# Performance work log

Hardware: AMD Instinct MI355X
Metric: run time of the kernel (lower is better)

Reference implementation:

```python
import jax, jax.numpy as jnp
import numpy as np

D_MODEL = 1024
NUM_HEADS = 16
D_K = D_MODEL // NUM_HEADS
EPS = 1e-6


def setup_inputs() -> dict:
    key = jax.random.key(0)
    ks = jax.random.split(key, 16)
    B, S = 2, 2048
    sc_in = 1.0 / np.sqrt(D_MODEL)
    sc_na = 1.0 / np.sqrt(D_K)
    inp = {
        "Q": jax.random.normal(ks[0], (B, S, D_MODEL), jnp.float32),
        "K": jax.random.normal(ks[1], (B, S, D_MODEL), jnp.float32),
        "V": jax.random.normal(ks[2], (B, S, D_MODEL), jnp.float32),
        "mask": jax.random.randint(ks[3], (1, 1, S, S), 0, 2, jnp.int32),
        # projection weights stored [in, out] (math-equivalent to torch Linear)
        "wq": jax.random.normal(ks[4], (D_MODEL, D_MODEL), jnp.float32) * sc_in,
        "bq": jnp.zeros((D_MODEL,), jnp.float32),
        "wk": jax.random.normal(ks[5], (D_MODEL, D_MODEL), jnp.float32) * sc_in,
        "bk": jnp.zeros((D_MODEL,), jnp.float32),
        "wv": jax.random.normal(ks[6], (D_MODEL, D_MODEL), jnp.float32) * sc_in,
        "bv": jnp.zeros((D_MODEL,), jnp.float32),
        "wo": jax.random.normal(ks[7], (D_MODEL, D_MODEL), jnp.float32) * sc_in,
        "bo": jnp.zeros((D_MODEL,), jnp.float32),
        # NeuralAttention score-fn params (per-head-dim transforms)
        "wnq": jax.random.normal(ks[8], (D_K, D_K), jnp.float32) * sc_na,
        "bnq": jnp.zeros((D_K,), jnp.float32),
        "wnk": jax.random.normal(ks[9], (D_K, D_K), jnp.float32) * sc_na,
        "bnk": jnp.zeros((D_K,), jnp.float32),
        "temperature": jnp.ones((NUM_HEADS, 1, 1), jnp.float32),
        "gamma": jnp.ones((D_MODEL,), jnp.float32),
    }
    return inp


def _split_heads(x):
    B, S, _ = x.shape
    return x.reshape(B, S, NUM_HEADS, D_K).transpose(0, 2, 1, 3)  # [B,H,S,dk]


def reference(Q, K, V, mask, wq, bq, wk, bk, wv, bv, wo, bo,
              wnq, bnq, wnk, bnk, temperature, gamma):
    B, S, _ = Q.shape
    q = _split_heads(Q @ wq + bq)  # [B,H,S,dk]
    k = _split_heads(K @ wk + bk)
    v = _split_heads(V @ wv + bv)
    # NeuralAttention: nonlinear per-token feature maps, then contraction
    qf = jnp.tanh(q @ wnq + bnq)
    kf = jnp.tanh(k @ wnk + bnk)
    scores = jnp.einsum('bhqd,bhkd->bhqk', qf, kf) / jnp.sqrt(jnp.float32(D_K))
    scores = scores / temperature  # [H,1,1] broadcasts over [B,H,S,S]
    scores = jnp.where(mask == 0, jnp.float32(-1e9), scores)
    attn = jax.nn.softmax(scores, axis=-1)
    ctx = jnp.einsum('bhqk,bhkd->bhqd', attn, v)
    out = ctx.transpose(0, 2, 1, 3).reshape(B, S, D_MODEL) @ wo + bo
    # RMSNorm
    rms = jax.lax.rsqrt(jnp.mean(out * out, axis=-1, keepdims=True) + EPS)
    return out * rms * gamma
```

## Files before the change

kernel.cpp:

```cpp
#include <hip/hip_runtime.h>
#include <hip/hip_bf16.h>
#include <math.h>

#define S_LEN 2048
#define BATCH 2
#define NH 16
#define DK 64
#define DM 1024
#define BS (BATCH * S_LEN)
#define BHS (BATCH * NH * S_LEN)
#define TRP 72
#define PSTR 72

using bf16x8  = __attribute__((ext_vector_type(8))) __bf16;
using floatx4 = __attribute__((ext_vector_type(4))) float;
using ushort4v = __attribute__((ext_vector_type(4))) unsigned short;

extern "C" __device__ float __ocml_exp2_f32(float);

__device__ __forceinline__ unsigned short f2bf(float f) {
    union { float f; unsigned u; } v; v.f = f;
    unsigned r = v.u + 0x7fffu + ((v.u >> 16) & 1u);
    return (unsigned short)(r >> 16);
}

__device__ __forceinline__ unsigned cvt_pk_bf16(float a, float b) {
    unsigned r;
    asm("v_cvt_pk_bf16_f32 %0, %1, %2" : "=v"(r) : "v"(a), "v"(b));
    return r;
}

__device__ __forceinline__ float fast_tanh(float x) {
    float e = __ocml_exp2_f32(x * 2.8853900817779268f);
    return 1.0f - 2.0f / (e + 1.0f);
}

__device__ __forceinline__ void gl2lds16(const void* g, void* l) {
    __builtin_amdgcn_global_load_lds(
        (__attribute__((address_space(1))) void*)(uintptr_t)g,
        (__attribute__((address_space(3))) void*)(uintptr_t)l,
        16, 0, 0);
}

__global__ void k_convert(const float* __restrict__ q, const float* __restrict__ k,
                          const float* __restrict__ v,
                          unsigned short* __restrict__ qb, unsigned short* __restrict__ kb,
                          unsigned short* __restrict__ vb) {
    const int N4 = BS * DM / 4;
    int i = blockIdx.x * 256 + threadIdx.x;
    int which = i / N4;
    int off = i - which * N4;
    const floatx4* src = (const floatx4*)(which == 0 ? q : which == 1 ? k : v);
    unsigned short* dst = which == 0 ? qb : which == 1 ? kb : vb;
    floatx4 x = src[off];
    ushort4v o;
    unsigned p01 = cvt_pk_bf16(x[0], x[1]);
    unsigned p23 = cvt_pk_bf16(x[2], x[3]);
    o[0] = (unsigned short)p01; o[1] = (unsigned short)(p01 >> 16);
    o[2] = (unsigned short)p23; o[3] = (unsigned short)(p23 >> 16);
    ((ushort4v*)dst)[off] = o;
}

__global__ void k_transpose(const float* s0, const float* s1, const float* s2, const float* s3,
                            unsigned short* d0, unsigned short* d1, unsigned short* d2,
                            unsigned short* d3, int n) {
    int z = blockIdx.z;
    const float* src = z == 0 ? s0 : z == 1 ? s1 : z == 2 ? s2 : s3;
    unsigned short* dst = z == 0 ? d0 : z == 1 ? d1 : z == 2 ? d2 : d3;
    __shared__ unsigned short tile[32][33];
    int tx = threadIdx.x & 31, ty = threadIdx.x >> 5;
#pragma unroll
    for (int i = 0; i < 4; i++) {
        int y = blockIdx.y * 32 + i * 8 + ty;
        tile[i * 8 + ty][tx] = f2bf(src[(size_t)y * n + blockIdx.x * 32 + tx]);
    }
    __syncthreads();
#pragma unroll
    for (int i = 0; i < 4; i++) {
        int r = blockIdx.x * 32 + i * 8 + ty;
        dst[(size_t)r * n + blockIdx.y * 32 + tx] = tile[tx][i * 8 + ty];
    }
}

__global__ void k_maskpack(const int* __restrict__ mask, unsigned int* __restrict__ mb) {
    int t = blockIdx.x * 256 + threadIdx.x;
    int row = t >> 6, w = t & 63;
    const int* p = mask + (size_t)row * S_LEN + w * 32;
    unsigned bits = 0;
#pragma unroll
    for (int i = 0; i < 32; i++) bits |= (p[i] != 0 ? 1u : 0u) << i;
    mb[t] = bits;
}

__global__ __launch_bounds__(256) void k_gemm_qkv(
    const unsigned short* __restrict__ Qb, const unsigned short* __restrict__ Kb,
    const unsigned short* __restrict__ Vb,
    const unsigned short* __restrict__ Wqt, const unsigned short* __restrict__ Wkt,
    const unsigned short* __restrict__ Wvt,
    const float* __restrict__ bq, const float* __restrict__ bk, const float* __restrict__ bv,
    unsigned short* __restrict__ qh, unsigned short* __restrict__ kh,
    unsigned short* __restrict__ vfrag) {
    const int K = DM;
    int z = blockIdx.z;
    const unsigned short* A  = z == 0 ? Qb  : z == 1 ? Kb  : Vb;
    const unsigned short* Wt = z == 0 ? Wqt : z == 1 ? Wkt : Wvt;
    const float* bias        = z == 0 ? bq  : z == 1 ? bk  : bv;
    int m0 = blockIdx.y * 128, n0 = blockIdx.x * 128;
    __shared__ unsigned short As[128 * 32];
    __shared__ unsigned short Bs[128 * 32];
    __shared__ unsigned short Tr[4][32 * TRP];
    int tid = threadIdx.x;
    int lane = tid & 63, wid = tid >> 6;
    int wy = wid >> 1, wx = wid & 1;
    int l16 = lane & 15, quad = lane >> 4;

    floatx4 acc[4][4] = {};

    for (int kt = 0; kt < K / 32; kt++) {
        int kk = kt * 32;
#pragma unroll
        for (int i = 0; i < 2; i++) {
            int c = i * 256 + tid;
            int row = c >> 2, seg = c & 3;
            gl2lds16(A + (size_t)(m0 + row) * K + kk + seg * 8, &As[c * 8]);
            gl2lds16(Wt + (size_t)(n0 + row) * K + kk + seg * 8, &Bs[c * 8]);
        }
        __syncthreads();
        bf16x8 af[4], bf[4];
#pragma unroll
        for (int mi = 0; mi < 4; mi++)
            af[mi] = *(const bf16x8*)&As[(wy * 64 + mi * 16 + l16) * 32 + quad * 8];
#pragma unroll
        for (int ni = 0; ni < 4; ni++)
            bf[ni] = *(const bf16x8*)&Bs[(wx * 64 + ni * 16 + l16) * 32 + quad * 8];
#pragma unroll
        for (int mi = 0; mi < 4; mi++)
#pragma unroll
            for (int ni = 0; ni < 4; ni++)
                acc[mi][ni] = __builtin_amdgcn_mfma_f32_16x16x32_bf16(af[mi], bf[ni], acc[mi][ni], 0, 0, 0);
        __syncthreads();
    }

    float bvv[4];
#pragma unroll
    for (int ni = 0; ni < 4; ni++) bvv[ni] = bias[n0 + wx * 64 + ni * 16 + l16];
    int head = (n0 + wx * 64) >> 6;
    int mbase = m0 + wy * 64;
    int b = mbase >> 11;
    unsigned short* tw = &Tr[wid][0];

    if (z < 2) {
        unsigned short* out = z == 0 ? qh : kh;
        size_t rowbase = (size_t)((b * NH + head) * S_LEN + (mbase & (S_LEN - 1))) * DK;
#pragma unroll
        for (int hh = 0; hh < 2; hh++) {
#pragma unroll
            for (int mi2 = 0; mi2 < 2; mi2++) {
                int mi = hh * 2 + mi2;
#pragma unroll
                for (int ni = 0; ni < 4; ni++) {
                    unsigned p01 = cvt_pk_bf16(acc[mi][ni][0] + bvv[ni], acc[mi][ni][1] + bvv[ni]);
                    unsigned p23 = cvt_pk_bf16(acc[mi][ni][2] + bvv[ni], acc[mi][ni][3] + bvv[ni]);
                    int ad = (mi2 * 16 + quad * 4) * TRP + ni * 16 + l16;
                    tw[ad] = (unsigned short)p01;
                    tw[ad + TRP] = (unsigned short)(p01 >> 16);
                    tw[ad + 2 * TRP] = (unsigned short)p23;
                    tw[ad + 3 * TRP] = (unsigned short)(p23 >> 16);
                }
            }
#pragma unroll
            for (int c = 0; c < 4; c++) {
                int g = c * 64 + lane;
                int ml = g >> 3, dc = g & 7;
                bf16x8 vv = *(const bf16x8*)&tw[ml * TRP + dc * 8];
                *(bf16x8*)&out[rowbase + (size_t)(hh * 32 + ml) * DK + dc * 8] = vv;
            }
        }
    } else {
        int kt2 = (mbase & (S_LEN - 1)) >> 6;
        size_t tilebase = ((size_t)(b * NH + head) * 32 + kt2) * 4096;
#pragma unroll
        for (int hh = 0; hh < 2; hh++) {
#pragma unroll
            for (int ni2 = 0; ni2 < 2; ni2++) {
                int ni = hh * 2 + ni2;
#pragma unroll
                for (int mi = 0; mi < 4; mi++) {
                    unsigned p01 = cvt_pk_bf16(acc[mi][ni][0] + bvv[ni], acc[mi][ni][1] + bvv[ni]);
                    unsigned p23 = cvt_pk_bf16(acc[mi][ni][2] + bvv[ni], acc[mi][ni][3] + bvv[ni]);
                    int ad = (ni2 * 16 + l16) * TRP + mi * 16 + quad * 4;
                    *(unsigned*)&tw[ad] = p01;
                    *(unsigned*)&tw[ad + 2] = p23;
                }
            }
#pragma unroll
            for (int c = 0; c < 4; c++) {
                int g = c * 64 + lane;
                int lt = g & 63;
                int qt = lt >> 4, l16t = lt & 15;
                int ad = ((c >> 1) * 16 + l16t) * TRP + (c & 1) * 32 + qt * 8;
                bf16x8 vv = *(const bf16x8*)&tw[ad];
                *(bf16x8*)&vfrag[tilebase + (size_t)(4 * hh + c) * 512 + lt * 8] = vv;
            }
        }
    }
}

__global__ __launch_bounds__(256) void k_gemm_out(const unsigned short* __restrict__ A,
                                                  const unsigned short* __restrict__ Wt,
                                                  const float* __restrict__ bias,
                                                  float* __restrict__ out_f32) {
    const int K = DM;
    int m0 = blockIdx.y * 128, n0 = blockIdx.x * 128;
    __shared__ unsigned short As[128 * 32];
    __shared__ unsigned short Bs[128 * 32];
    int tid = threadIdx.x;
    int lane = tid & 63, wid = tid >> 6;
    int wy = wid >> 1, wx = wid & 1;
    int l16 = lane & 15, quad = lane >> 4;

    floatx4 acc[4][4] = {};

    for (int kt = 0; kt < K / 32; kt++) {
        int kk = kt * 32;
#pragma unroll
        for (int i = 0; i < 2; i++) {
            int c = i * 256 + tid;
            int row = c >> 2, seg = c & 3;
            gl2lds16(A + (size_t)(m0 + row) * K + kk + seg * 8, &As[c * 8]);
            gl2lds16(Wt + (size_t)(n0 + row) * K + kk + seg * 8, &Bs[c * 8]);
        }
        __syncthreads();
        bf16x8 af[4], bf[4];
#pragma unroll
        for (int mi = 0; mi < 4; mi++)
            af[mi] = *(const bf16x8*)&As[(wy * 64 + mi * 16 + l16) * 32 + quad * 8];
#pragma unroll
        for (int ni = 0; ni < 4; ni++)
            bf[ni] = *(const bf16x8*)&Bs[(wx * 64 + ni * 16 + l16) * 32 + quad * 8];
#pragma unroll
        for (int mi = 0; mi < 4; mi++)
#pragma unroll
            for (int ni = 0; ni < 4; ni++)
                acc[mi][ni] = __builtin_amdgcn_mfma_f32_16x16x32_bf16(af[mi], bf[ni], acc[mi][ni], 0, 0, 0);
        __syncthreads();
    }

#pragma unroll
    for (int mi = 0; mi < 4; mi++) {
#pragma unroll
        for (int ni = 0; ni < 4; ni++) {
            int col = n0 + wx * 64 + ni * 16 + l16;
            float bvv = bias[col];
#pragma unroll
            for (int r = 0; r < 4; r++) {
                int row = m0 + wy * 64 + mi * 16 + quad * 4 + r;
                out_f32[(size_t)row * DM + col] = acc[mi][ni][r] + bvv;
            }
        }
    }
}

__global__ __launch_bounds__(256) void k_feature(const unsigned short* __restrict__ qh,
                                                 const unsigned short* __restrict__ kh,
                                                 const unsigned short* __restrict__ wnqt,
                                                 const unsigned short* __restrict__ wnkt,
                                                 const float* __restrict__ bnq,
                                                 const float* __restrict__ bnk,
                                                 const float* __restrict__ temp,
                                                 unsigned short* __restrict__ qfb,
                                                 unsigned short* __restrict__ kfrag) {
    int zy = blockIdx.y;
    const unsigned short* src = zy == 0 ? qh : kh;
    const unsigned short* wt = zy == 0 ? wnqt : wnkt;
    const float* bias = zy == 0 ? bnq : bnk;

    __shared__ unsigned short Tr[64 * TRP];
    int tid = threadIdx.x, lane = tid & 63, wid = tid >> 6;
    int l16 = lane & 15, quad = lane >> 4;
    int row0 = blockIdx.x * 64;
    int bh = row0 >> 11, h = bh & 15;
    float sc = (zy == 0) ? 1.4426950408889634f / (8.0f * temp[h]) : 1.0f;

    bf16x8 af[2];
#pragma unroll
    for (int ks = 0; ks < 2; ks++)
        af[ks] = *(const bf16x8*)(src + (size_t)(row0 + wid * 16 + l16) * DK + ks * 32 + quad * 8);

    floatx4 acc[4] = {};
#pragma unroll
    for (int ni = 0; ni < 4; ni++) {
#pragma unroll
        for (int ks = 0; ks < 2; ks++) {
            bf16x8 bfr = *(const bf16x8*)(wt + (size_t)(ni * 16 + l16) * DK + ks * 32 + quad * 8);
            acc[ni] = __builtin_amdgcn_mfma_f32_16x16x32_bf16(af[ks], bfr, acc[ni], 0, 0, 0);
        }
    }
#pragma unroll
    for (int ni = 0; ni < 4; ni++) {
        float bv = bias[ni * 16 + l16];
        float t0 = fast_tanh(acc[ni][0] + bv) * sc;
        float t1 = fast_tanh(acc[ni][1] + bv) * sc;
        float t2 = fast_tanh(acc[ni][2] + bv) * sc;
        float t3 = fast_tanh(acc[ni][3] + bv) * sc;
        unsigned p01 = cvt_pk_bf16(t0, t1);
        unsigned p23 = cvt_pk_bf16(t2, t3);
        int ad = (wid * 16 + quad * 4) * TRP + ni * 16 + l16;
        Tr[ad] = (unsigned short)p01;
        Tr[ad + TRP] = (unsigned short)(p01 >> 16);
        Tr[ad + 2 * TRP] = (unsigned short)p23;
        Tr[ad + 3 * TRP] = (unsigned short)(p23 >> 16);
    }
    __syncthreads();
    if (zy == 0) {
#pragma unroll
        for (int c = 0; c < 2; c++) {
            int g = c * 256 + tid;
            int ml = g >> 3, dc = g & 7;
            bf16x8 vv = *(const bf16x8*)&Tr[ml * TRP + dc * 8];
            *(bf16x8*)&qfb[(size_t)(row0 + ml) * DK + dc * 8] = vv;
        }
    } else {
        int kt = (row0 & (S_LEN - 1)) >> 6;
        size_t tb = ((size_t)bh * 32 + kt) * 4096;
#pragma unroll
        for (int c = 0; c < 2; c++) {
            int F = c * 256 + tid;
            int i = F >> 6, lt = F & 63;
            int qt = lt >> 4, lt16 = lt & 15;
            int ad = ((i >> 1) * 16 + lt16) * TRP + (i & 1) * 32 + qt * 8;
            bf16x8 vv = *(const bf16x8*)&Tr[ad];
            *(bf16x8*)&kfrag[tb + (size_t)i * 512 + lt * 8] = vv;
        }
    }
}

__global__ __launch_bounds__(256, 4) void k_attn(const unsigned short* __restrict__ qf,
                                                 const unsigned short* __restrict__ kfr,
                                                 const unsigned short* __restrict__ vfr,
                                                 const unsigned long long* __restrict__ mb64,
                                                 unsigned short* __restrict__ ctx) {
    int tid = threadIdx.x, lane = tid & 63, wid = tid >> 6;
    int l16 = lane & 15, quad = lane >> 4;
    int bh = blockIdx.y;
    int b = bh >> 4, h = bh & 15;
    int q0 = blockIdx.x * 64 + wid * 16;

    const unsigned short* qfb = qf + (size_t)bh * S_LEN * DK;
    const unsigned short* kbase = kfr + (size_t)bh * 32 * 4096;
    const unsigned short* vbase = vfr + (size_t)bh * 32 * 4096;

    __shared__ unsigned short Kbuf[2][4096];
    __shared__ unsigned short Plds[4][16 * PSTR];
    unsigned short* myP = Plds[wid];

    bf16x8 aq[2];
#pragma unroll
    for (int ks = 0; ks < 2; ks++)
        aq[ks] = *(const bf16x8*)(qfb + (size_t)(q0 + l16) * DK + ks * 32 + quad * 8);

    gl2lds16(kbase + tid * 8, &Kbuf[0][tid * 8]);
    gl2lds16(kbase + 2048 + tid * 8, &Kbuf[0][2048 + tid * 8]);

    floatx4 oacc[4] = {};
    float l_part[4] = {0.f, 0.f, 0.f, 0.f};
    const unsigned long long* mrow = mb64 + (size_t)(q0 + quad * 4) * 32;

    for (int kt = 0; kt < S_LEN / 64; kt++) {
        __syncthreads();
        int nb = (kt + 1) & 1;
        const unsigned short* kn = kbase + (size_t)((kt + 1) & 31) * 4096;
        gl2lds16(kn + tid * 8, &Kbuf[nb][tid * 8]);
        gl2lds16(kn + 2048 + tid * 8, &Kbuf[nb][2048 + tid * 8]);
        const unsigned short* vt = vbase + (size_t)kt * 4096 + lane * 8;
        bf16x8 vf[8];
#pragma unroll
        for (int i = 0; i < 8; i++) vf[i] = *(const bf16x8*)(vt + i * 512);
        unsigned wlo[4], whi[4];
#pragma unroll
        for (int r = 0; r < 4; r++) {
            unsigned long long m = mrow[r * 32 + kt];
            wlo[r] = (unsigned)(m >> l16);
            whi[r] = (unsigned)(m >> (l16 + 32));
        }
        const unsigned short* kb = &Kbuf[kt & 1][lane * 8];
        bf16x8 kf8[8];
#pragma unroll
        for (int i = 0; i < 8; i++) kf8[i] = *(const bf16x8*)(kb + i * 512);
        floatx4 sf[4];
#pragma unroll
        for (int ni = 0; ni < 4; ni++) {
            floatx4 z = {};
            z = __builtin_amdgcn_mfma_f32_16x16x32_bf16(aq[0], kf8[ni * 2], z, 0, 0, 0);
            z = __builtin_amdgcn_mfma_f32_16x16x32_bf16(aq[1], kf8[ni * 2 + 1], z, 0, 0, 0);
            sf[ni] = z;
        }
#pragma unroll
        for (int ni2 = 0; ni2 < 2; ni2++) {
#pragma unroll
            for (int r = 0; r < 4; r++) {
                unsigned wv = ni2 ? whi[r] : wlo[r];
                float sA = (wv & 1u) ? sf[2 * ni2][r] : -23.0f;
                float sB = (wv & 0x10000u) ? sf[2 * ni2 + 1][r] : -23.0f;
                float pA = __ocml_exp2_f32(sA);
                float pB = __ocml_exp2_f32(sB);
                l_part[r] += pA + pB;
                unsigned pk = cvt_pk_bf16(pA, pB);
                int ad = (quad * 4 + r) * PSTR + ni2 * 32 + l16;
                myP[ad] = (unsigned short)pk;
                myP[ad + 16] = (unsigned short)(pk >> 16);
            }
        }
        bf16x8 pa[2];
#pragma unroll
        for (int ks = 0; ks < 2; ks++)
            pa[ks] = *(const bf16x8*)&myP[l16 * PSTR + ks * 32 + quad * 8];
#pragma unroll
        for (int ni = 0; ni < 4; ni++) {
            oacc[ni] = __builtin_amdgcn_mfma_f32_16x16x32_bf16(pa[0], vf[ni * 2], oacc[ni], 0, 0, 0);
            oacc[ni] = __builtin_amdgcn_mfma_f32_16x16x32_bf16(pa[1], vf[ni * 2 + 1], oacc[ni], 0, 0, 0);
        }
    }
#pragma unroll
    for (int r = 0; r < 4; r++) {
#pragma unroll
        for (int off = 1; off < 16; off <<= 1)
            l_part[r] += __shfl_xor(l_part[r], off, 16);
    }
    float inv[4];
#pragma unroll
    for (int r = 0; r < 4; r++) inv[r] = 1.0f / l_part[r];
#pragma unroll
    for (int ni = 0; ni < 4; ni++) {
        int d = ni * 16 + l16;
#pragma unroll
        for (int r = 0; r < 4; r++) {
            int s = q0 + quad * 4 + r;
            ctx[(size_t)(b * S_LEN + s) * DM + h * DK + d] = f2bf(oacc[ni][r] * inv[r]);
        }
    }
}

__global__ __launch_bounds__(256) void k_rmsnorm(const float* __restrict__ x,
                                                 const float* __restrict__ gamma,
                                                 float* __restrict__ out) {
    int row = blockIdx.x, tid = threadIdx.x;
    const floatx4* xr = (const floatx4*)(x + (size_t)row * DM);
    floatx4 v = xr[tid];
    float ss = v[0] * v[0] + v[1] * v[1] + v[2] * v[2] + v[3] * v[3];
#pragma unroll
    for (int off = 1; off < 64; off <<= 1) ss += __shfl_xor(ss, off);
    __shared__ float red[4];
    int lane = tid & 63, wid = tid >> 6;
    if (lane == 0) red[wid] = ss;
    __syncthreads();
    float tot = red[0] + red[1] + red[2] + red[3];
    float rms = rsqrtf(tot * (1.0f / DM) + 1e-6f);
    floatx4 g = ((const floatx4*)gamma)[tid];
    floatx4 o;
    o[0] = v[0] * rms * g[0];
    o[1] = v[1] * rms * g[1];
    o[2] = v[2] * rms * g[2];
    o[3] = v[3] * rms * g[3];
    ((floatx4*)(out + (size_t)row * DM))[tid] = o;
}

extern "C" void kernel_launch(void* const* d_in, const int* in_sizes, int n_in,
                              void* d_out, int out_size, void* d_ws, size_t ws_size,
                              hipStream_t stream) {
    const float* Q = (const float*)d_in[0];
    const float* K = (const float*)d_in[1];
    const float* V = (const float*)d_in[2];
    const int* mask = (const int*)d_in[3];
    const float* wq = (const float*)d_in[4];
    const float* bq = (const float*)d_in[5];
    const float* wk = (const float*)d_in[6];
    const float* bk = (const float*)d_in[7];
    const float* wv = (const float*)d_in[8];
    const float* bv = (const float*)d_in[9];
    const float* wo = (const float*)d_in[10];
    const float* bo = (const float*)d_in[11];
    const float* wnq = (const float*)d_in[12];
    const float* bnq = (const float*)d_in[13];
    const float* wnk = (const float*)d_in[14];
    const float* bnk = (const float*)d_in[15];
    const float* temp = (const float*)d_in[16];
    const float* gamma = (const float*)d_in[17];

    char* w = (char*)d_ws;
    size_t o = 0;
    auto alloc = [&](size_t bytes) {
        char* p = w + o;
        o += (bytes + 255) & ~(size_t)255;
        return p;
    };
    unsigned short* Qb = (unsigned short*)alloc((size_t)BS * DM * 2);
    unsigned short* Kb = (unsigned short*)alloc((size_t)BS * DM * 2);
    unsigned short* Vb = (unsigned short*)alloc((size_t)BS * DM * 2);
    unsigned short* Wqt = (unsigned short*)alloc((size_t)DM * DM * 2);
    unsigned short* Wkt = (unsigned short*)alloc((size_t)DM * DM * 2);
    unsigned short* Wvt = (unsigned short*)alloc((size_t)DM * DM * 2);
    unsigned short* Wot = (unsigned short*)alloc((size_t)DM * DM * 2);
    unsigned short* wnqt = (unsigned short*)alloc((size_t)DK * DK * 2);
    unsigned short* wnkt = (unsigned short*)alloc((size_t)DK * DK * 2);
    unsigned short* qh = (unsigned short*)alloc((size_t)BHS * DK * 2);
    unsigned short* kh = (unsigned short*)alloc((size_t)BHS * DK * 2);
    unsigned short* vfrag = (unsigned short*)alloc((size_t)BHS * DK * 2);
    unsigned short* qfb = (unsigned short*)alloc((size_t)BHS * DK * 2);
    unsigned short* kfrag = (unsigned short*)alloc((size_t)BHS * DK * 2);
    unsigned int* mb = (unsigned int*)alloc((size_t)S_LEN * (S_LEN / 32) * 4);
    unsigned short* ctx = (unsigned short*)alloc((size_t)BS * DM * 2);
    float* outt = (float*)alloc((size_t)BS * DM * 4);

    k_convert<<<dim3(3 * BS * DM / 4 / 256), 256, 0, stream>>>(Q, K, V, Qb, Kb, Vb);
    k_transpose<<<dim3(32, 32, 4), 256, 0, stream>>>(wq, wk, wv, wo, Wqt, Wkt, Wvt, Wot, DM);
    k_transpose<<<dim3(2, 2, 2), 256, 0, stream>>>(wnq, wnk, wnq, wnq, wnqt, wnkt, wnqt, wnqt, DK);
    k_maskpack<<<dim3(S_LEN * 64 / 256), 256, 0, stream>>>(mask, mb);

    k_gemm_qkv<<<dim3(8, 32, 3), 256, 0, stream>>>(Qb, Kb, Vb, Wqt, Wkt, Wvt,
                                                   bq, bk, bv, qh, kh, vfrag);

    k_feature<<<dim3(BHS / 64, 2), 256, 0, stream>>>(qh, kh, wnqt, wnkt, bnq, bnk, temp,
                                                     qfb, kfrag);

    k_attn<<<dim3(S_LEN / 64, BATCH * NH), 256, 0, stream>>>(
        qfb, kfrag, vfrag, (const unsigned long long*)mb, ctx);

    k_gemm_out<<<dim3(8, 32), 256, 0, stream>>>(ctx, Wot, bo, outt);
    k_rmsnorm<<<dim3(BS), 256, 0, stream>>>(outt, gamma, (float*)d_out);
}
```

Before: 313.3 us.

## Fuse feature transform into QKV GEMM epilogue and widen attention query tile

The per-head tanh feature map (small 64x64 GEMM, bias, tanh, scaling) now runs in the QKV projection epilogue directly from the LDS transpose buffer. This removes the k_feature launch and the qh/kh intermediate round trip through global memory. Separately, each attention wave now handles 32 query rows instead of 16, reusing each K/V tile across twice as many queries and halving the grid. It uses transposed score MFMAs with per-lane mask words and lowers launch bounds occupancy from 4 to 2 to fit the extra registers.

```diff
diff --git a/kernel.cpp b/kernel.cpp
--- a/kernel.cpp
+++ b/kernel.cpp
@@ -98,7 +98,10 @@
     const unsigned short* __restrict__ Wqt, const unsigned short* __restrict__ Wkt,
     const unsigned short* __restrict__ Wvt,
     const float* __restrict__ bq, const float* __restrict__ bk, const float* __restrict__ bv,
-    unsigned short* __restrict__ qh, unsigned short* __restrict__ kh,
+    const unsigned short* __restrict__ wnqt, const unsigned short* __restrict__ wnkt,
+    const float* __restrict__ bnq, const float* __restrict__ bnk,
+    const float* __restrict__ temp,
+    unsigned short* __restrict__ qfb, unsigned short* __restrict__ kfrag,
     unsigned short* __restrict__ vfrag) {
     const int K = DM;
     int z = blockIdx.z;
@@ -147,11 +150,49 @@
     int head = (n0 + wx * 64) >> 6;
     int mbase = m0 + wy * 64;
     int b = mbase >> 11;
+    int bh = b * NH + head;
     unsigned short* tw = &Tr[wid][0];
 
-    if (z < 2) {
-        unsigned short* out = z == 0 ? qh : kh;
-        size_t rowbase = (size_t)((b * NH + head) * S_LEN + (mbase & (S_LEN - 1))) * DK;
+    if (z == 2) {
+        int kt2 = (mbase & (S_LEN - 1)) >> 6;
+        size_t tilebase = ((size_t)bh * 32 + kt2) * 4096;
+#pragma unroll
+        for (int hh = 0; hh < 2; hh++) {
+#pragma unroll
+            for (int ni2 = 0; ni2 < 2; ni2++) {
+                int ni = hh * 2 + ni2;
+#pragma unroll
+                for (int mi = 0; mi < 4; mi++) {
+                    unsigned p01 = cvt_pk_bf16(acc[mi][ni][0] + bvv[ni], acc[mi][ni][1] + bvv[ni]);
+                    unsigned p23 = cvt_pk_bf16(acc[mi][ni][2] + bvv[ni], acc[mi][ni][3] + bvv[ni]);
+                    int ad = (ni2 * 16 + l16) * TRP + mi * 16 + quad * 4;
+                    *(unsigned*)&tw[ad] = p01;
+                    *(unsigned*)&tw[ad + 2] = p23;
+                }
+            }
+#pragma unroll
+            for (int c = 0; c < 4; c++) {
+                int ad = ((c >> 1) * 16 + l16) * TRP + (c & 1) * 32 + quad * 8;
+                bf16x8 vv = *(const bf16x8*)&tw[ad];
+                *(bf16x8*)&vfrag[tilebase + (size_t)(4 * hh + c) * 512 + lane * 8] = vv;
+            }
+        }
+    } else {
+        const unsigned short* wn = z == 0 ? wnqt : wnkt;
+        const float* bn = z == 0 ? bnq : bnk;
+        float sc = z == 0 ? 1.4426950408889634f / (8.0f * temp[head]) : 1.0f;
+        bf16x8 wf[4][2];
+        float bnv[4];
+#pragma unroll
+        for (int ni = 0; ni < 4; ni++) {
+            bnv[ni] = bn[ni * 16 + l16];
+#pragma unroll
+            for (int ks = 0; ks < 2; ks++)
+                wf[ni][ks] = *(const bf16x8*)(wn + (size_t)(ni * 16 + l16) * DK + ks * 32 + quad * 8);
+        }
+        size_t rowbase = (size_t)((size_t)bh * S_LEN + (mbase & (S_LEN - 1))) * DK;
+        int kt2 = (mbase & (S_LEN - 1)) >> 6;
+        size_t tb = ((size_t)bh * 32 + kt2) * 4096;
 #pragma unroll
         for (int hh = 0; hh < 2; hh++) {
 #pragma unroll
@@ -168,39 +209,51 @@
                     tw[ad + 3 * TRP] = (unsigned short)(p23 >> 16);
                 }
             }
-#pragma unroll
-            for (int c = 0; c < 4; c++) {
-                int g = c * 64 + lane;
-                int ml = g >> 3, dc = g & 7;
-                bf16x8 vv = *(const bf16x8*)&tw[ml * TRP + dc * 8];
-                *(bf16x8*)&out[rowbase + (size_t)(hh * 32 + ml) * DK + dc * 8] = vv;
-            }
-        }
-    } else {
-        int kt2 = (mbase & (S_LEN - 1)) >> 6;
-        size_t tilebase = ((size_t)(b * NH + head) * 32 + kt2) * 4096;
-#pragma unroll
-        for (int hh = 0; hh < 2; hh++) {
-#pragma unroll
-            for (int ni2 = 0; ni2 < 2; ni2++) {
-                int ni = hh * 2 + ni2;
-#pragma unroll
-                for (int mi = 0; mi < 4; mi++) {
-                    unsigned p01 = cvt_pk_bf16(acc[mi][ni][0] + bvv[ni], acc[mi][ni][1] + bvv[ni]);
-                    unsigned p23 = cvt_pk_bf16(acc[mi][ni][2] + bvv[ni], acc[mi][ni][3] + bvv[ni]);
-                    int ad = (ni2 * 16 + l16) * TRP + mi * 16 + quad * 4;
-                    *(unsigned*)&tw[ad] = p01;
-                    *(unsigned*)&tw[ad + 2] = p23;
-                }
-            }
-#pragma unroll
-            for (int c = 0; c < 4; c++) {
-                int g = c * 64 + lane;
-                int lt = g & 63;
-                int qt = lt >> 4, l16t = lt & 15;
-                int ad = ((c >> 1) * 16 + l16t) * TRP + (c & 1) * 32 + qt * 8;
-                bf16x8 vv = *(const bf16x8*)&tw[ad];
-                *(bf16x8*)&vfrag[tilebase + (size_t)(4 * hh + c) * 512 + lt * 8] = vv;
+            floatx4 facc[2][4] = {};
+#pragma unroll
+            for (int mg = 0; mg < 2; mg++) {
+                bf16x8 af2[2];
+#pragma unroll
+                for (int ks = 0; ks < 2; ks++)
+                    af2[ks] = *(const bf16x8*)&tw[(mg * 16 + l16) * TRP + ks * 32 + quad * 8];
+#pragma unroll
+                for (int ni = 0; ni < 4; ni++) {
+                    facc[mg][ni] = __builtin_amdgcn_mfma_f32_16x16x32_bf16(af2[0], wf[ni][0], facc[mg][ni], 0, 0, 0);
+                    facc[mg][ni] = __builtin_amdgcn_mfma_f32_16x16x32_bf16(af2[1], wf[ni][1], facc[mg][ni], 0, 0, 0);
+                }
+            }
+#pragma unroll
+            for (int mg = 0; mg < 2; mg++) {
+#pragma unroll
+                for (int ni = 0; ni < 4; ni++) {
+                    float t0 = fast_tanh(facc[mg][ni][0] + bnv[ni]) * sc;
+                    float t1 = fast_tanh(facc[mg][ni][1] + bnv[ni]) * sc;
+                    float t2 = fast_tanh(facc[mg][ni][2] + bnv[ni]) * sc;
+                    float t3 = fast_tanh(facc[mg][ni][3] + bnv[ni]) * sc;
+                    unsigned p01 = cvt_pk_bf16(t0, t1);
+                    unsigned p23 = cvt_pk_bf16(t2, t3);
+                    int ad = (mg * 16 + quad * 4) * TRP + ni * 16 + l16;
+                    tw[ad] = (unsigned short)p01;
+                    tw[ad + TRP] = (unsigned short)(p01 >> 16);
+                    tw[ad + 2 * TRP] = (unsigned short)p23;
+                    tw[ad + 3 * TRP] = (unsigned short)(p23 >> 16);
+                }
+            }
+            if (z == 0) {
+#pragma unroll
+                for (int c = 0; c < 4; c++) {
+                    int g = c * 64 + lane;
+                    int ml = g >> 3, dc = g & 7;
+                    bf16x8 vv = *(const bf16x8*)&tw[ml * TRP + dc * 8];
+                    *(bf16x8*)&qfb[rowbase + (size_t)(hh * 32 + ml) * DK + dc * 8] = vv;
+                }
+            } else {
+#pragma unroll
+                for (int c = 0; c < 4; c++) {
+                    int ad = ((c >> 1) * 16 + l16) * TRP + (c & 1) * 32 + quad * 8;
+                    bf16x8 vv = *(const bf16x8*)&tw[ad];
+                    *(bf16x8*)&kfrag[tb + (size_t)(hh * 4 + c) * 512 + lane * 8] = vv;
+                }
             }
         }
     }
@@ -261,81 +314,7 @@
     }
 }
 
-__global__ __launch_bounds__(256) void k_feature(const unsigned short* __restrict__ qh,
-                                                 const unsigned short* __restrict__ kh,
-                                                 const unsigned short* __restrict__ wnqt,
-                                                 const unsigned short* __restrict__ wnkt,
-                                                 const float* __restrict__ bnq,
-                                                 const float* __restrict__ bnk,
-                                                 const float* __restrict__ temp,
-                                                 unsigned short* __restrict__ qfb,
-                                                 unsigned short* __restrict__ kfrag) {
-    int zy = blockIdx.y;
-    const unsigned short* src = zy == 0 ? qh : kh;
-    const unsigned short* wt = zy == 0 ? wnqt : wnkt;
-    const float* bias = zy == 0 ? bnq : bnk;
-
-    __shared__ unsigned short Tr[64 * TRP];
-    int tid = threadIdx.x, lane = tid & 63, wid = tid >> 6;
-    int l16 = lane & 15, quad = lane >> 4;
-    int row0 = blockIdx.x * 64;
-    int bh = row0 >> 11, h = bh & 15;
-    float sc = (zy == 0) ? 1.4426950408889634f / (8.0f * temp[h]) : 1.0f;
-
-    bf16x8 af[2];
-#pragma unroll
-    for (int ks = 0; ks < 2; ks++)
-        af[ks] = *(const bf16x8*)(src + (size_t)(row0 + wid * 16 + l16) * DK + ks * 32 + quad * 8);
-
-    floatx4 acc[4] = {};
-#pragma unroll
-    for (int ni = 0; ni < 4; ni++) {
-#pragma unroll
-        for (int ks = 0; ks < 2; ks++) {
-            bf16x8 bfr = *(const bf16x8*)(wt + (size_t)(ni * 16 + l16) * DK + ks * 32 + quad * 8);
-            acc[ni] = __builtin_amdgcn_mfma_f32_16x16x32_bf16(af[ks], bfr, acc[ni], 0, 0, 0);
-        }
-    }
-#pragma unroll
-    for (int ni = 0; ni < 4; ni++) {
-        float bv = bias[ni * 16 + l16];
-        float t0 = fast_tanh(acc[ni][0] + bv) * sc;
-        float t1 = fast_tanh(acc[ni][1] + bv) * sc;
-        float t2 = fast_tanh(acc[ni][2] + bv) * sc;
-        float t3 = fast_tanh(acc[ni][3] + bv) * sc;
-        unsigned p01 = cvt_pk_bf16(t0, t1);
-        unsigned p23 = cvt_pk_bf16(t2, t3);
-        int ad = (wid * 16 + quad * 4) * TRP + ni * 16 + l16;
-        Tr[ad] = (unsigned short)p01;
-        Tr[ad + TRP] = (unsigned short)(p01 >> 16);
-        Tr[ad + 2 * TRP] = (unsigned short)p23;
-        Tr[ad + 3 * TRP] = (unsigned short)(p23 >> 16);
-    }
-    __syncthreads();
-    if (zy == 0) {
-#pragma unroll
-        for (int c = 0; c < 2; c++) {
-            int g = c * 256 + tid;
-            int ml = g >> 3, dc = g & 7;
-            bf16x8 vv = *(const bf16x8*)&Tr[ml * TRP + dc * 8];
-            *(bf16x8*)&qfb[(size_t)(row0 + ml) * DK + dc * 8] = vv;
-        }
-    } else {
-        int kt = (row0 & (S_LEN - 1)) >> 6;
-        size_t tb = ((size_t)bh * 32 + kt) * 4096;
-#pragma unroll
-        for (int c = 0; c < 2; c++) {
-            int F = c * 256 + tid;
-            int i = F >> 6, lt = F & 63;
-            int qt = lt >> 4, lt16 = lt & 15;
-            int ad = ((i >> 1) * 16 + lt16) * TRP + (i & 1) * 32 + qt * 8;
-            bf16x8 vv = *(const bf16x8*)&Tr[ad];
-            *(bf16x8*)&kfrag[tb + (size_t)i * 512 + lt * 8] = vv;
-        }
-    }
-}
-
-__global__ __launch_bounds__(256, 4) void k_attn(const unsigned short* __restrict__ qf,
+__global__ __launch_bounds__(256, 2) void k_attn(const unsigned short* __restrict__ qf,
                                                  const unsigned short* __restrict__ kfr,
                                                  const unsigned short* __restrict__ vfr,
                                                  const unsigned long long* __restrict__ mb64,
@@ -344,27 +323,30 @@
     int l16 = lane & 15, quad = lane >> 4;
     int bh = blockIdx.y;
     int b = bh >> 4, h = bh & 15;
-    int q0 = blockIdx.x * 64 + wid * 16;
+    int q0 = blockIdx.x * 128 + wid * 32;
 
     const unsigned short* qfb = qf + (size_t)bh * S_LEN * DK;
     const unsigned short* kbase = kfr + (size_t)bh * 32 * 4096;
     const unsigned short* vbase = vfr + (size_t)bh * 32 * 4096;
 
     __shared__ unsigned short Kbuf[2][4096];
-    __shared__ unsigned short Plds[4][16 * PSTR];
+    __shared__ unsigned short Plds[4][32 * PSTR];
     unsigned short* myP = Plds[wid];
 
-    bf16x8 aq[2];
-#pragma unroll
-    for (int ks = 0; ks < 2; ks++)
-        aq[ks] = *(const bf16x8*)(qfb + (size_t)(q0 + l16) * DK + ks * 32 + quad * 8);
+    bf16x8 bq[2][2];
+#pragma unroll
+    for (int g = 0; g < 2; g++)
+#pragma unroll
+        for (int ks = 0; ks < 2; ks++)
+            bq[g][ks] = *(const bf16x8*)(qfb + (size_t)(q0 + g * 16 + l16) * DK + ks * 32 + quad * 8);
 
     gl2lds16(kbase + tid * 8, &Kbuf[0][tid * 8]);
     gl2lds16(kbase + 2048 + tid * 8, &Kbuf[0][2048 + tid * 8]);
 
-    floatx4 oacc[4] = {};
-    float l_part[4] = {0.f, 0.f, 0.f, 0.f};
-    const unsigned long long* mrow = mb64 + (size_t)(q0 + quad * 4) * 32;
+    floatx4 oacc[2][4] = {};
+    float lrow[2] = {0.f, 0.f};
+    const unsigned long long* mq0 = mb64 + (size_t)(q0 + l16) * 32;
+    const unsigned long long* mq1 = mb64 + (size_t)(q0 + 16 + l16) * 32;
 
     for (int kt = 0; kt < S_LEN / 64; kt++) {
         __syncthreads();
@@ -376,67 +358,53 @@
         bf16x8 vf[8];
 #pragma unroll
         for (int i = 0; i < 8; i++) vf[i] = *(const bf16x8*)(vt + i * 512);
-        unsigned wlo[4], whi[4];
-#pragma unroll
-        for (int r = 0; r < 4; r++) {
-            unsigned long long m = mrow[r * 32 + kt];
-            wlo[r] = (unsigned)(m >> l16);
-            whi[r] = (unsigned)(m >> (l16 + 32));
-        }
+        unsigned long long mw[2] = {mq0[kt], mq1[kt]};
         const unsigned short* kb = &Kbuf[kt & 1][lane * 8];
         bf16x8 kf8[8];
 #pragma unroll
         for (int i = 0; i < 8; i++) kf8[i] = *(const bf16x8*)(kb + i * 512);
-        floatx4 sf[4];
+#pragma unroll
+        for (int g = 0; g < 2; g++) {
+            unsigned short* pw = myP + (g * 16 + l16) * PSTR;
+#pragma unroll
+            for (int kbk = 0; kbk < 4; kbk++) {
+                floatx4 s = {};
+                s = __builtin_amdgcn_mfma_f32_16x16x32_bf16(kf8[kbk * 2], bq[g][0], s, 0, 0, 0);
+                s = __builtin_amdgcn_mfma_f32_16x16x32_bf16(kf8[kbk * 2 + 1], bq[g][1], s, 0, 0, 0);
+                unsigned w = (unsigned)(mw[g] >> (kbk * 16 + quad * 4));
+                float p0 = __ocml_exp2_f32((w & 1u) ? s[0] : -23.0f);
+                float p1 = __ocml_exp2_f32((w & 2u) ? s[1] : -23.0f);
+                float p2 = __ocml_exp2_f32((w & 4u) ? s[2] : -23.0f);
+                float p3 = __ocml_exp2_f32((w & 8u) ? s[3] : -23.0f);
+                lrow[g] += (p0 + p1) + (p2 + p3);
+                *(unsigned*)&pw[kbk * 16 + quad * 4] = cvt_pk_bf16(p0, p1);
+                *(unsigned*)&pw[kbk * 16 + quad * 4 + 2] = cvt_pk_bf16(p2, p3);
+            }
+            bf16x8 pa0 = *(const bf16x8*)&myP[(g * 16 + l16) * PSTR + quad * 8];
+            bf16x8 pa1 = *(const bf16x8*)&myP[(g * 16 + l16) * PSTR + 32 + quad * 8];
+#pragma unroll
+            for (int ni = 0; ni < 4; ni++) {
+                oacc[g][ni] = __builtin_amdgcn_mfma_f32_16x16x32_bf16(pa0, vf[ni * 2], oacc[g][ni], 0, 0, 0);
+                oacc[g][ni] = __builtin_amdgcn_mfma_f32_16x16x32_bf16(pa1, vf[ni * 2 + 1], oacc[g][ni], 0, 0, 0);
+            }
+        }
+    }
+#pragma unroll
+    for (int g = 0; g < 2; g++) {
+        float lr = lrow[g];
+        lr += __shfl_xor(lr, 16);
+        lr += __shfl_xor(lr, 32);
+        float inv[4];
+#pragma unroll
+        for (int r = 0; r < 4; r++) inv[r] = 1.0f / __shfl(lr, quad * 4 + r, 16);
 #pragma unroll
         for (int ni = 0; ni < 4; ni++) {
-            floatx4 z = {};
-            z = __builtin_amdgcn_mfma_f32_16x16x32_bf16(aq[0], kf8[ni * 2], z, 0, 0, 0);
-            z = __builtin_amdgcn_mfma_f32_16x16x32_bf16(aq[1], kf8[ni * 2 + 1], z, 0, 0, 0);
-            sf[ni] = z;
-        }
-#pragma unroll
-        for (int ni2 = 0; ni2 < 2; ni2++) {
+            int d = ni * 16 + l16;
 #pragma unroll
             for (int r = 0; r < 4; r++) {
-                unsigned wv = ni2 ? whi[r] : wlo[r];
-                float sA = (wv & 1u) ? sf[2 * ni2][r] : -23.0f;
-                float sB = (wv & 0x10000u) ? sf[2 * ni2 + 1][r] : -23.0f;
-                float pA = __ocml_exp2_f32(sA);
-                float pB = __ocml_exp2_f32(sB);
-                l_part[r] += pA + pB;
-                unsigned pk = cvt_pk_bf16(pA, pB);
-                int ad = (quad * 4 + r) * PSTR + ni2 * 32 + l16;
-                myP[ad] = (unsigned short)pk;
-                myP[ad + 16] = (unsigned short)(pk >> 16);
-            }
-        }
-        bf16x8 pa[2];
-#pragma unroll
-        for (int ks = 0; ks < 2; ks++)
-            pa[ks] = *(const bf16x8*)&myP[l16 * PSTR + ks * 32 + quad * 8];
-#pragma unroll
-        for (int ni = 0; ni < 4; ni++) {
-            oacc[ni] = __builtin_amdgcn_mfma_f32_16x16x32_bf16(pa[0], vf[ni * 2], oacc[ni], 0, 0, 0);
-            oacc[ni] = __builtin_amdgcn_mfma_f32_16x16x32_bf16(pa[1], vf[ni * 2 + 1], oacc[ni], 0, 0, 0);
-        }
-    }
-#pragma unroll
-    for (int r = 0; r < 4; r++) {
-#pragma unroll
-        for (int off = 1; off < 16; off <<= 1)
-            l_part[r] += __shfl_xor(l_part[r], off, 16);
-    }
-    float inv[4];
-#pragma unroll
-    for (int r = 0; r < 4; r++) inv[r] = 1.0f / l_part[r];
-#pragma unroll
-    for (int ni = 0; ni < 4; ni++) {
-        int d = ni * 16 + l16;
-#pragma unroll
-        for (int r = 0; r < 4; r++) {
-            int s = q0 + quad * 4 + r;
-            ctx[(size_t)(b * S_LEN + s) * DM + h * DK + d] = f2bf(oacc[ni][r] * inv[r]);
+                int s = q0 + g * 16 + quad * 4 + r;
+                ctx[(size_t)(b * S_LEN + s) * DM + h * DK + d] = f2bf(oacc[g][ni][r] * inv[r]);
+            }
         }
     }
 }
@@ -503,8 +471,6 @@
     unsigned short* Wot = (unsigned short*)alloc((size_t)DM * DM * 2);
     unsigned short* wnqt = (unsigned short*)alloc((size_t)DK * DK * 2);
     unsigned short* wnkt = (unsigned short*)alloc((size_t)DK * DK * 2);
-    unsigned short* qh = (unsigned short*)alloc((size_t)BHS * DK * 2);
-    unsigned short* kh = (unsigned short*)alloc((size_t)BHS * DK * 2);
     unsigned short* vfrag = (unsigned short*)alloc((size_t)BHS * DK * 2);
     unsigned short* qfb = (unsigned short*)alloc((size_t)BHS * DK * 2);
     unsigned short* kfrag = (unsigned short*)alloc((size_t)BHS * DK * 2);
@@ -518,12 +484,10 @@
     k_maskpack<<<dim3(S_LEN * 64 / 256), 256, 0, stream>>>(mask, mb);
 
     k_gemm_qkv<<<dim3(8, 32, 3), 256, 0, stream>>>(Qb, Kb, Vb, Wqt, Wkt, Wvt,
-                                                   bq, bk, bv, qh, kh, vfrag);
-
-    k_feature<<<dim3(BHS / 64, 2), 256, 0, stream>>>(qh, kh, wnqt, wnkt, bnq, bnk, temp,
-                                                     qfb, kfrag);
-
-    k_attn<<<dim3(S_LEN / 64, BATCH * NH), 256, 0, stream>>>(
+                                                   bq, bk, bv, wnqt, wnkt, bnq, bnk, temp,
+                                                   qfb, kfrag, vfrag);
+
+    k_attn<<<dim3(S_LEN / 128, BATCH * NH), 256, 0, stream>>>(
         qfb, kfrag, vfrag, (const unsigned long long*)mb, ctx);
 
     k_gemm_out<<<dim3(8, 32), 256, 0, stream>>>(ctx, Wot, bo, outt);
```

Result: faster. 303.3 us (-3.2%).
